# Kernel optimization log

Hardware: AMD Instinct MI355X
Metric: run time of the kernel (lower is better)

## Reference

```python
import jax, jax.numpy as jnp
import numpy as np

B, T, S = 16, 300, 160
N_MELS, PRE, ENC, ATT, LOC, K, DIM = 80, 256, 512, 128, 32, 31, 1024


def setup_inputs() -> dict:
    key = jax.random.key(0)
    ks = jax.random.split(key, 26)

    def rn(k, shape, fan_in):
        return (jax.random.normal(k, shape) / np.sqrt(fan_in)).astype(jnp.float32)

    inp = {}
    inp['mels'] = jax.random.normal(ks[0], (B, N_MELS, T), dtype=jnp.float32)
    inp['enc_out'] = jax.random.normal(ks[1], (B, S, ENC), dtype=jnp.float32)
    inp['text_len'] = jax.random.randint(ks[2], (B,), S // 2, S + 1).astype(jnp.int32)
    # attention params
    inp['Wt'] = rn(ks[3], (ATT, ENC), ENC)          # lin_target
    inp['Wq'] = rn(ks[4], (ATT, DIM), DIM)          # lin_query
    inp['w_score'] = rn(ks[5], (ATT,), ATT)         # lin_score weight [1,ATT] -> vector
    inp['conv1'] = rn(ks[6], (LOC, 1, K), K)        # Conv1d(1, loc_dim, K)
    inp['conv2'] = rn(ks[7], (ATT, LOC, 1), LOC)    # Conv1d(loc_dim, ATT, 1)
    # prenet (1x1 convs == per-frame linears)
    inp['pW1'] = rn(ks[8], (PRE, N_MELS), N_MELS)
    inp['pb1'] = jnp.zeros((PRE,), jnp.float32)
    inp['pW2'] = rn(ks[9], (PRE, PRE), PRE)
    inp['pb2'] = jnp.zeros((PRE,), jnp.float32)
    # 2-layer LSTM cells (gate order i,f,g,o as in torch)
    inp['Wih0'] = rn(ks[10], (4 * DIM, PRE + ENC), PRE + ENC)
    inp['Whh0'] = rn(ks[11], (4 * DIM, DIM), DIM)
    inp['bih0'] = jnp.zeros((4 * DIM,), jnp.float32)
    inp['bhh0'] = jnp.zeros((4 * DIM,), jnp.float32)
    inp['Wih1'] = rn(ks[12], (4 * DIM, DIM), DIM)
    inp['Whh1'] = rn(ks[13], (4 * DIM, DIM), DIM)
    inp['bih1'] = jnp.zeros((4 * DIM,), jnp.float32)
    inp['bhh1'] = jnp.zeros((4 * DIM,), jnp.float32)
    inp['h0'] = (jax.random.normal(ks[14], (2, DIM)) * 0.05).astype(jnp.float32)
    inp['c0'] = (jax.random.normal(ks[15], (2, DIM)) * 0.05).astype(jnp.float32)
    # projection
    inp['projW'] = rn(ks[16], (N_MELS + 1, ENC + DIM), ENC + DIM)
    inp['projb'] = jnp.zeros((N_MELS + 1,), jnp.float32)
    return inp


def _lstm_cell(x, h, c, Wih, Whh, bih, bhh):
    g = x @ Wih.T + bih + h @ Whh.T + bhh
    i, f, gg, o = jnp.split(g, 4, axis=-1)
    c2 = jax.nn.sigmoid(f) * c + jax.nn.sigmoid(i) * jnp.tanh(gg)
    h2 = jax.nn.sigmoid(o) * jnp.tanh(c2)
    return h2, c2


def reference(mels, enc_out, text_len, Wt, Wq, w_score, conv1, conv2,
              pW1, pb1, pW2, pb2,
              Wih0, Whh0, bih0, bhh0, Wih1, Whh1, bih1, bhh1,
              h0, c0, projW, projb):
    Bv, n_mel, Tv = mels.shape
    Sv = enc_out.shape[1]
    Kv = conv1.shape[-1]
    # prenet over [go, mels] (dropout disabled: deterministic=True, eval)
    mels_cat = jnp.concatenate([jnp.zeros((Bv, n_mel, 1), mels.dtype), mels], axis=2)
    p = jax.nn.relu(jnp.einsum('od,bdt->bot', pW1, mels_cat) + pb1[None, :, None])
    p = jax.nn.relu(jnp.einsum('od,bot->bot'.replace('o','q',1).replace('d','o').replace('q','o',1), pW2, p) + pb2[None, :, None]) if False else jax.nn.relu(jnp.einsum('od,bdt->bot', pW2, p) + pb2[None, :, None])
    mel_pre = jnp.transpose(p[:, :, :Tv], (2, 0, 1))  # [T, B, PRE]
    l_enc = enc_out @ Wt.T  # [B, S, ATT]
    pad_mask = jnp.arange(Sv)[None, :] >= text_len[:, None]  # [B, S] True at pads

    def step(carry, mel_t):
        h0_, h1_, c0_, c1_, cum = carry
        # location features from cumulative attention [B, S]
        loc = jax.lax.conv_general_dilated(cum[:, None, :], conv1, (1,),
                                           [(Kv // 2, Kv // 2)],
                                           dimension_numbers=('NCH', 'OIH', 'NCH'))  # [B,LOC,S]
        loc = jnp.einsum('al,bls->bsa', conv2[:, :, 0], loc)  # [B, S, ATT]
        q = h1_ @ Wq.T  # [B, ATT]
        score = jnp.tanh(q[:, None, :] + l_enc + loc) @ w_score  # [B, S]
        score = jnp.where(pad_mask, -jnp.inf, score)
        attn = jax.nn.softmax(score, axis=1)  # [B, S]
        align = jnp.einsum('bs,bse->be', attn, enc_out)  # [B, ENC]
        x = jnp.concatenate([mel_t, align], axis=1)
        h0n, c0n = _lstm_cell(x, h0_, c0_, Wih0, Whh0, bih0, bhh0)
        h1n, c1n = _lstm_cell(h0n, h1_, c1_, Wih1, Whh1, bih1, bhh1)
        cell_out = jnp.concatenate([h1n, align], axis=1)
        return (h0n, h1n, c0n, c1n, cum + attn), (cell_out, attn)

    init = (jnp.broadcast_to(h0[0], (Bv, h0.shape[1])),
            jnp.broadcast_to(h0[1], (Bv, h0.shape[1])),
            jnp.broadcast_to(c0[0], (Bv, c0.shape[1])),
            jnp.broadcast_to(c0[1], (Bv, c0.shape[1])),
            jnp.zeros((Bv, Sv), mels.dtype))
    _, (cell_outs, attns) = jax.lax.scan(step, init, mel_pre)
    proj = cell_outs @ projW.T + projb  # [T, B, n_mel+1]
    mel_out = jnp.transpose(proj[..., :n_mel], (1, 2, 0))   # [B, n_mel, T]
    stop_out = jnp.transpose(proj[..., n_mel], (1, 0))      # [B, T]
    attn_scores = jnp.transpose(attns, (1, 2, 0))           # [B, S, T]
    return mel_out, stop_out, attn_scores
```

## Files before the change

kernel.cpp:

```cpp
#include <hip/hip_runtime.h>

#define T_    300
#define B_    16
#define S_    160
#define NMEL_ 80
#define PRE_  256
#define ENC_  512
#define ATT_  128
#define DIM_  1024

#define XST1  1288
#define XST2  520
#define XST3  1032
#define AOFF  16512
#define WLDS  20608
#define XTOT  36992
#define BARWORDS 17408

#define HSLOT (B_*DIM_)
#define ASLOT (B_*ENC_)
#define GSLOT (B_*256)

typedef unsigned int u32;
typedef unsigned short u16;

__device__ __forceinline__ float fexp2f(float x) { return __builtin_amdgcn_exp2f(x); }
__device__ __forceinline__ float fsigf(float x)  { return 1.0f / (1.0f + fexp2f(-1.442695041f * x)); }
__device__ __forceinline__ float ftanhf(float x) {
  float xc = fminf(fmaxf(x, -15.0f), 15.0f);
  float e = fexp2f(2.885390082f * xc);
  return (e - 1.0f) / (e + 1.0f);
}

__device__ __forceinline__ u16 f2bf(float f) {
  u32 b = __float_as_uint(f);
  return (u16)((b + 0x7fffu + ((b >> 16) & 1u)) >> 16);
}
__device__ __forceinline__ float4 bf4(const u16* p) {
  const uint2 u = *(const uint2*)p;
  float4 w;
  w.x = __uint_as_float(u.x << 16);
  w.y = __uint_as_float(u.x & 0xffff0000u);
  w.z = __uint_as_float(u.y << 16);
  w.w = __uint_as_float(u.y & 0xffff0000u);
  return w;
}

__device__ __forceinline__ float4 ld1q_sys(const float* p) {
  float4 v;
  asm volatile("global_load_dwordx4 %0, %1, off sc0 sc1\n\ts_waitcnt vmcnt(0)"
               : "=v"(v) : "v"(p) : "memory");
  return v;
}
__device__ __forceinline__ void st_sys(float* p, float v) {
  asm volatile("global_store_dword %0, %1, off sc0 sc1" :: "v"(p), "v"(v) : "memory");
}
__device__ __forceinline__ u32 ld_sys_u32(const u32* p) {
  u32 r;
  asm volatile("global_load_dword %0, %1, off sc0 sc1\n\ts_waitcnt vmcnt(0)"
               : "=v"(r) : "v"(p) : "memory");
  return r;
}
__device__ __forceinline__ void st_sys_u32(u32* p, u32 v) {
  asm volatile("global_store_dword %0, %1, off sc0 sc1" :: "v"(p), "v"(v) : "memory");
}

__device__ __forceinline__ void gridbar(u32* bar, int tid, int blk, u32 ep) {
  asm volatile("s_waitcnt vmcnt(0)" ::: "memory");
  __syncthreads();
  if (tid == 0) {
    const int g = blk & 15;
    u32* cnt  = bar + g*1024;
    u32* grel = bar + g*1024 + 64;
    u32* tcnt = bar + 16384;
    const u32 tgt = ep*16u + 15u;
    u32 old = __hip_atomic_fetch_add(cnt, 1u, __ATOMIC_RELAXED, __HIP_MEMORY_SCOPE_AGENT);
    if (old == tgt) {
      u32 told = __hip_atomic_fetch_add(tcnt, 1u, __ATOMIC_RELAXED, __HIP_MEMORY_SCOPE_AGENT);
      if (told == tgt) {
        #pragma unroll
        for (int g2 = 0; g2 < 16; ++g2) st_sys_u32(bar + g2*1024 + 64, ep + 1u);
      } else {
        while (ld_sys_u32(grel) != ep + 1u) __builtin_amdgcn_s_sleep(1);
      }
    } else {
      while (ld_sys_u32(grel) != ep + 1u) __builtin_amdgcn_s_sleep(1);
    }
  }
  __syncthreads();
}

#define DPP_ADD(v, ctrl, rmask) do { \
  int _t = __builtin_amdgcn_update_dpp(0, __float_as_int(v), (ctrl), (rmask), 0xf, false); \
  (v) += __int_as_float(_t); } while (0)

#define REDUCE64(v) do { \
  DPP_ADD(v, 0x111, 0xf); \
  DPP_ADD(v, 0x112, 0xf); \
  DPP_ADD(v, 0x114, 0xf); \
  DPP_ADD(v, 0x118, 0xf); \
  DPP_ADD(v, 0x142, 0xa); \
  DPP_ADD(v, 0x143, 0x8); } while (0)

__launch_bounds__(256)
__global__ void prenet_kernel(const float* __restrict__ mels,
                              const float* __restrict__ pW1, const float* __restrict__ pb1,
                              const float* __restrict__ pW2, const float* __restrict__ pb2,
                              float* __restrict__ melpre) {
  __shared__ float mcol[NMEL_];
  __shared__ float pcol[PRE_];
  const int b = blockIdx.x / 30;
  const int tbase = (blockIdx.x % 30) * 10;
  const int tid = threadIdx.x;
  for (int f = 0; f < 10; ++f) {
    const int t = tbase + f;
    if (tid < NMEL_) mcol[tid] = (t == 0) ? 0.0f : mels[(b*NMEL_ + tid)*T_ + (t-1)];
    __syncthreads();
    {
      float a1 = pb1[tid];
      const float* w1 = pW1 + tid*NMEL_;
      for (int m = 0; m < NMEL_; ++m) a1 += w1[m]*mcol[m];
      pcol[tid] = fmaxf(a1, 0.0f);
    }
    __syncthreads();
    {
      float a2 = pb2[tid];
      const float* w2 = pW2 + tid*PRE_;
      for (int d = 0; d < PRE_; d += 4) {
        const float4 wv = *(const float4*)(w2 + d);
        a2 += wv.x*pcol[d] + wv.y*pcol[d+1] + wv.z*pcol[d+2] + wv.w*pcol[d+3];
      }
      melpre[(t*B_ + b)*PRE_ + tid] = fmaxf(a2, 0.0f);
    }
    __syncthreads();
  }
}

__launch_bounds__(256)
__global__ void init_kernel(const float* __restrict__ h0,
                            const float* __restrict__ conv1, const float* __restrict__ conv2,
                            float* __restrict__ h1buf, float* __restrict__ h0st,
                            float* __restrict__ weff, u32* __restrict__ bar) {
  const int idx = blockIdx.x*256 + threadIdx.x;
  if (idx < B_*DIM_) {
    const int j = idx & (DIM_-1);
    h0st[idx]  = h0[j];
    h1buf[idx] = h0[DIM_ + j];
  } else if (idx < B_*DIM_ + ATT_*32) {
    const int r = idx - B_*DIM_;
    const int a = r >> 5, k = r & 31;
    float acc = 0.0f;
    if (k < 31) {
      for (int l = 0; l < 32; ++l) acc += conv2[a*32 + l]*conv1[l*31 + k];
    }
    weff[r] = acc;
  } else if (idx < B_*DIM_ + ATT_*32 + BARWORDS) {
    bar[idx - (B_*DIM_ + ATT_*32)] = 0u;
  }
}

__launch_bounds__(256)
__global__ void wcvt_kernel(const float* __restrict__ Wih0, const float* __restrict__ Whh0,
                            const float* __restrict__ Wih1, const float* __restrict__ Whh1,
                            const float* __restrict__ Wq,
                            u16* __restrict__ Wih0h, u16* __restrict__ Whh0h,
                            u16* __restrict__ Wih1h, u16* __restrict__ Whh1h,
                            u16* __restrict__ Wqh) {
  const int n0 = 4096*768, n1 = 4096*1024, nq = ATT_*DIM_;
  const int stride = gridDim.x*256;
  for (int i = blockIdx.x*256 + threadIdx.x; i < n0; i += stride) Wih0h[i] = f2bf(Wih0[i]);
  for (int i = blockIdx.x*256 + threadIdx.x; i < n1; i += stride) {
    Whh0h[i] = f2bf(Whh0[i]);
    Wih1h[i] = f2bf(Wih1[i]);
    Whh1h[i] = f2bf(Whh1[i]);
  }
  for (int i = blockIdx.x*256 + threadIdx.x; i < nq; i += stride) Wqh[i] = f2bf(Wq[i]);
}

__launch_bounds__(256)
__global__ void lenc_kernel(const float* __restrict__ enc, const float* __restrict__ Wt,
                            float* __restrict__ lencb) {
  __shared__ float es[4*ENC_];
  const int b = blockIdx.x / 40;
  const int s0 = (blockIdx.x % 40) * 4;
  const int tid = threadIdx.x;
  for (int idx = tid; idx < 4*ENC_; idx += 256) es[idx] = enc[(b*S_ + s0)*ENC_ + idx];
  __syncthreads();
  const int a = tid & 127, sh = tid >> 7;
  const float* w = Wt + a*ENC_;
  for (int p = 0; p < 2; ++p) {
    const int sl = sh*2 + p;
    const float* e = es + sl*ENC_;
    float acc = 0.0f;
    for (int j = 0; j < ENC_; j += 4) {
      const float4 wv = *(const float4*)(w + j);
      acc += wv.x*e[j] + wv.y*e[j+1] + wv.z*e[j+2] + wv.w*e[j+3];
    }
    lencb[(b*S_ + s0 + sl)*ATT_ + a] = acc;
  }
}

__launch_bounds__(512, 1)
__global__ void decoder_kernel(
    const float* __restrict__ melpre, const float* __restrict__ lencb,
    const float* __restrict__ weff,
    float* __restrict__ h1buf, float* __restrict__ albuf, float* __restrict__ h0st,
    float* __restrict__ g0pre, float* __restrict__ g1pre, u32* __restrict__ bar,
    const float* __restrict__ enc, const int* __restrict__ tlen,
    const u16* __restrict__ Wqh, const float* __restrict__ wsc,
    const u16* __restrict__ Wih0h, const u16* __restrict__ Whh0h,
    const u16* __restrict__ Wih1h, const u16* __restrict__ Whh1h,
    const float* __restrict__ bih0, const float* __restrict__ bhh0,
    const float* __restrict__ bih1, const float* __restrict__ bhh1,
    const float* __restrict__ c0in, const float* __restrict__ projW, const float* __restrict__ projb,
    float* __restrict__ out_mel, float* __restrict__ out_stop, float* __restrict__ out_attn)
{
  extern __shared__ float xt[];
  __shared__ float red_s[1];
  __shared__ float gv[256];
  __shared__ float gv0[256];
  __shared__ float gv1[256];
  __shared__ float q_s[ATT_];
  __shared__ float spf[S_*4];
  __shared__ float score_s[S_];
  __shared__ float attn_s[S_];
  __shared__ float bsum_s[2][20];

  float* const cum_p = xt + AOFF;
  float* const projx = xt + AOFF + 192;
  float* const wscs  = xt + AOFF + 1728;
  u16* const wl = (u16*)(xt + WLDS);

  const int blk = blockIdx.x;
  const int tid = threadIdx.x;
  const int ks = tid & 63;
  const int bgb = ((tid >> 6) & 1)*8;
  const int rg = tid >> 7;
  const int j0 = blk*4;
  const bool hg0 = (blk >= 16 && blk < 80);
  const bool hg1 = (blk >= 80 && blk < 144);
  const int jx0 = blk - 16;
  const int jx1 = blk - 80;

  float c0r = 0.0f, c1r = 0.0f;
  if (tid < 64) {
    const int j = j0 + (tid >> 4);
    c0r = c0in[j];
    c1r = c0in[DIM_ + j];
  }
  int mylen = 0;
  if (blk < B_) {
    mylen = tlen[blk];
    for (int i = tid; i < S_ + 30; i += 512) cum_p[i] = 0.0f;
    if (tid < ATT_) wscs[tid] = wsc[tid];
  } else {
    for (int i = tid; i < 8192; i += 512) {
      const int c = i >> 6, l = i & 63;
      const int m = c >> 6, cm = c & 63;
      const int ri = cm >> 4, rgw = (cm >> 2) & 3, q = cm & 3;
      const u16* src = (m ? Whh1h : Wih1h) + (ri*1024 + j0 + rgw)*1024 + q*256 + l*4;
      *(uint2*)(wl + c*256 + l*4) = *(const uint2*)src;
    }
    if (tid < 16) {
      const int ri = tid >> 2, rgw = tid & 3;
      const int n = ri*1024 + j0 + rgw;
      bsum_s[0][tid] = bih0[n] + bhh0[n];
      bsum_s[1][tid] = bih1[n] + bhh1[n];
    } else if (tid < 20) {
      const int rgw = tid - 16;
      const int n0 = rgw*1024 + ((jx0 < 64) ? jx0 : 0);
      const int n1 = rgw*1024 + (hg1 ? jx1 : 0);
      bsum_s[0][16 + rgw] = bih0[n0] + bhh0[n0];
      bsum_s[1][16 + rgw] = bih1[n1] + bhh1[n1];
    }
  }
  __syncthreads();

  u32 ep = 0;

  for (int t = 0; t < T_; ++t) {
    if (blk < B_) {
      const int b = blk;
      if (tid < 256) {
        *(float4*)(projx + tid*4) =
            *(const float4*)(h1buf + t*HSLOT + b*DIM_ + tid*4);
      } else if (tid < 384) {
        const int j = tid - 256;
        const int ap = (t > 0) ? (t-1) : 0;
        *(float4*)(projx + 1024 + j*4) =
            *(const float4*)(albuf + ap*ASLOT + b*ENC_ + j*4);
      }
      __syncthreads();
      {
        const int a = tid & 127, part = tid >> 7;
        const float* hp = projx + part*256;
        const u16* wq = Wqh + a*DIM_ + part*256;
        float acc = 0.0f;
        for (int j = 0; j < 256; j += 4) {
          const float4 wv = bf4(wq + j);
          const float4 hv = *(const float4*)(hp + j);
          acc += wv.x*hv.x + wv.y*hv.y + wv.z*hv.z + wv.w*hv.w;
        }
        spf[a*4 + part] = acc;
      }
      __syncthreads();
      if (tid < ATT_) q_s[tid] = spf[tid*4] + spf[tid*4+1] + spf[tid*4+2] + spf[tid*4+3];
      __syncthreads();
      {
        const int sl = tid & 127, ag = tid >> 7;
        const int a0 = ag*32;
        #pragma unroll
        for (int p = 0; p < 2; ++p) {
          const int s = sl + p*128;
          if (s < S_) {
            float cw[32];
            #pragma unroll
            for (int k = 0; k < 31; ++k) cw[k] = cum_p[s + k];
            cw[31] = 0.0f;
            const float* le = lencb + (b*S_ + s)*ATT_ + a0;
            const float* wr = weff + a0*32;
            float ps = 0.0f;
            for (int i4 = 0; i4 < 8; ++i4) {
              const float4 lev = *(const float4*)(le + i4*4);
              #pragma unroll
              for (int ii = 0; ii < 4; ++ii) {
                const int i = i4*4 + ii;
                const float4* wk4 = (const float4*)(wr + i*32);
                float loc = 0.0f;
                #pragma unroll
                for (int kq = 0; kq < 8; ++kq) {
                  const float4 wv = wk4[kq];
                  loc += wv.x*cw[kq*4+0] + wv.y*cw[kq*4+1] + wv.z*cw[kq*4+2] + wv.w*cw[kq*4+3];
                }
                const float lef = (ii==0)?lev.x:(ii==1)?lev.y:(ii==2)?lev.z:lev.w;
                ps += wscs[a0 + i]*ftanhf(q_s[a0 + i] + lef + loc);
              }
            }
            spf[s*4 + ag] = ps;
          }
        }
      }
      __syncthreads();
      if (tid < S_) {
        float sc = spf[tid*4] + spf[tid*4+1] + spf[tid*4+2] + spf[tid*4+3];
        if (tid >= mylen) sc = -1.0e30f;
        score_s[tid] = sc;
      }
      __syncthreads();
      if (tid < 64) {
        float m = -1.0e30f;
        for (int i = tid; i < S_; i += 64) m = fmaxf(m, score_s[i]);
        #pragma unroll
        for (int o = 32; o > 0; o >>= 1) m = fmaxf(m, __shfl_xor(m, o, 64));
        float sum = 0.0f;
        for (int i = tid; i < S_; i += 64) {
          const float e = fexp2f(1.442695041f*(score_s[i] - m));
          score_s[i] = e;
          sum += e;
        }
        #pragma unroll
        for (int o = 32; o > 0; o >>= 1) sum += __shfl_xor(sum, o, 64);
        if (tid == 0) red_s[0] = sum;
      }
      __syncthreads();
      {
        const float inv = 1.0f / red_s[0];
        if (tid < S_) {
          const float av = score_s[tid]*inv;
          attn_s[tid] = av;
          cum_p[15 + tid] += av;
          out_attn[(b*S_ + tid)*T_ + t] = av;
        }
      }
      __syncthreads();
      {
        const float* eb = enc + (b*S_)*ENC_ + tid;
        float acc = 0.0f;
        for (int s = 0; s < S_; ++s) acc += attn_s[s]*eb[s*ENC_];
        st_sys(albuf + t*ASLOT + b*ENC_ + tid, acc);
      }
    } else {
      for (int i = tid; i < 1024; i += 512) {
        float4 v = *(const float4*)(melpre + t*4096 + i*4);
        *(float4*)(xt + (i>>6)*XST1 + (i&63)*4) = v;
      }
      {
        const float* src = h0st + t*HSLOT;
        float4 r[8];
        #pragma unroll
        for (int u = 0; u < 8; ++u) r[u] = *(const float4*)(src + (tid + u*512)*4);
        #pragma unroll
        for (int u = 0; u < 8; ++u) {
          const int i = tid + u*512;
          *(float4*)(xt + (i>>8)*XST1 + 256 + (i&255)*4) = r[u];
        }
      }
      __syncthreads();
      {
        const int nr = hg0 ? 5 : 4;
        int nrow[5];
        #pragma unroll
        for (int ri = 0; ri < 4; ++ri) nrow[ri] = ri*1024 + j0 + rg;
        nrow[4] = rg*1024 + ((jx0 < 64) ? jx0 : 0);
        #pragma unroll
        for (int hf = 0; hf < 2; ++hf) {
          const int b0 = bgb + hf*4;
          float acc[5][4];
          #pragma unroll
          for (int ri = 0; ri < 5; ++ri)
            #pragma unroll
            for (int bi = 0; bi < 4; ++bi) acc[ri][bi] = 0.0f;
          {
            const int j = ks*4;
            float4 w4[5];
            #pragma unroll
            for (int ri = 0; ri < 5; ++ri)
              if (ri < nr) w4[ri] = bf4(Wih0h + nrow[ri]*768 + j);
            #pragma unroll
            for (int bi = 0; bi < 4; ++bi) {
              const float4 xv = *(const float4*)(xt + (b0+bi)*XST1 + j);
              #pragma unroll
              for (int ri = 0; ri < 5; ++ri)
                if (ri < nr)
                  acc[ri][bi] += w4[ri].x*xv.x + w4[ri].y*xv.y + w4[ri].z*xv.z + w4[ri].w*xv.w;
            }
          }
          #pragma unroll
          for (int q = 0; q < 4; ++q) {
            const int j = q*256 + ks*4;
            float4 w4[5];
            #pragma unroll
            for (int ri = 0; ri < 5; ++ri)
              if (ri < nr) w4[ri] = bf4(Whh0h + nrow[ri]*1024 + j);
            #pragma unroll
            for (int bi = 0; bi < 4; ++bi) {
              const float4 xv = *(const float4*)(xt + (b0+bi)*XST1 + 256 + j);
              #pragma unroll
              for (int ri = 0; ri < 5; ++ri)
                if (ri < nr)
                  acc[ri][bi] += w4[ri].x*xv.x + w4[ri].y*xv.y + w4[ri].z*xv.z + w4[ri].w*xv.w;
            }
          }
          #pragma unroll
          for (int ri = 0; ri < 5; ++ri)
            if (ri < nr)
              #pragma unroll
              for (int bi = 0; bi < 4; ++bi) {
                float v = acc[ri][bi];
                REDUCE64(v);
                if (ks == 63) {
                  v += (ri < 4) ? bsum_s[0][ri*4 + rg] : bsum_s[0][16 + rg];
                  if (ri < 4) gv0[(ri*4 + rg)*16 + (b0+bi)] = v;
                  else        st_sys(g0pre + t*GSLOT + (b0+bi)*256 + jx0*4 + rg, v);
                }
              }
        }
      }
      __syncthreads();
      {
        const float* src = h1buf + t*HSLOT;
        float4 r[8];
        #pragma unroll
        for (int u = 0; u < 8; ++u) r[u] = *(const float4*)(src + (tid + u*512)*4);
        #pragma unroll
        for (int u = 0; u < 8; ++u) {
          const int i = tid + u*512;
          *(float4*)(xt + (i>>8)*XST1 + (i&255)*4) = r[u];
        }
      }
      __syncthreads();
      {
        const int nr = hg1 ? 5 : 4;
        const int nprox = rg*1024 + (hg1 ? jx1 : 0);
        #pragma unroll
        for (int hf = 0; hf < 2; ++hf) {
          const int b0 = bgb + hf*4;
          float acc[5][4];
          #pragma unroll
          for (int ri = 0; ri < 5; ++ri)
            #pragma unroll
            for (int bi = 0; bi < 4; ++bi) acc[ri][bi] = 0.0f;
          #pragma unroll
          for (int q = 0; q < 4; ++q) {
            const int j = q*256 + ks*4;
            float4 w4[5];
            #pragma unroll
            for (int ri = 0; ri < 4; ++ri)
              w4[ri] = bf4(wl + (64 + (ri*4 + rg)*4 + q)*256 + ks*4);
            if (nr == 5) w4[4] = bf4(Whh1h + nprox*1024 + j);
            #pragma unroll
            for (int bi = 0; bi < 4; ++bi) {
              const float4 xv = *(const float4*)(xt + (b0+bi)*XST1 + j);
              #pragma unroll
              for (int ri = 0; ri < 5; ++ri)
                if (ri < nr)
                  acc[ri][bi] += w4[ri].x*xv.x + w4[ri].y*xv.y + w4[ri].z*xv.z + w4[ri].w*xv.w;
            }
          }
          #pragma unroll
          for (int ri = 0; ri < 5; ++ri)
            if (ri < nr)
              #pragma unroll
              for (int bi = 0; bi < 4; ++bi) {
                float v = acc[ri][bi];
                REDUCE64(v);
                if (ks == 63) {
                  v += (ri < 4) ? bsum_s[1][ri*4 + rg] : bsum_s[1][16 + rg];
                  if (ri < 4) gv1[(ri*4 + rg)*16 + (b0+bi)] = v;
                  else        st_sys(g1pre + t*GSLOT + (b0+bi)*256 + jx1*4 + rg, v);
                }
              }
        }
      }
    }
    gridbar(bar, tid, blk, ep); ++ep;

    {
      {
        const float* src = albuf + t*ASLOT;
        float4 r[4];
        #pragma unroll
        for (int u = 0; u < 4; ++u) r[u] = *(const float4*)(src + (tid + u*512)*4);
        #pragma unroll
        for (int u = 0; u < 4; ++u) {
          const int i = tid + u*512;
          *(float4*)(xt + (i>>7)*XST2 + (i&127)*4) = r[u];
        }
      }
      __syncthreads();
      float acc[4][8];
      #pragma unroll
      for (int ri = 0; ri < 4; ++ri)
        #pragma unroll
        for (int bi = 0; bi < 8; ++bi) acc[ri][bi] = 0.0f;
      #pragma unroll
      for (int q = 0; q < 2; ++q) {
        const int j = q*256 + ks*4;
        float4 w4[4];
        #pragma unroll
        for (int ri = 0; ri < 4; ++ri)
          w4[ri] = bf4(Wih0h + (ri*1024 + j0 + rg)*768 + 256 + j);
        #pragma unroll
        for (int bi = 0; bi < 8; ++bi) {
          const float4 xv = *(const float4*)(xt + (bgb+bi)*XST2 + j);
          #pragma unroll
          for (int ri = 0; ri < 4; ++ri)
            acc[ri][bi] += w4[ri].x*xv.x + w4[ri].y*xv.y + w4[ri].z*xv.z + w4[ri].w*xv.w;
        }
      }
      #pragma unroll
      for (int ri = 0; ri < 4; ++ri)
        #pragma unroll
        for (int bi = 0; bi < 8; ++bi) {
          float v = acc[ri][bi];
          REDUCE64(v);
          if (ks == 63) gv[(rg*4 + ri)*16 + (bgb+bi)] = v;
        }
      __syncthreads();
      if (tid < 64) {
        const int jl = tid >> 4, bb = tid & 15;
        const int j = j0 + jl;
        float pi, pf, pg, po;
        if (blk < B_) {
          const float4 g4 = *(const float4*)(g0pre + t*GSLOT + bb*256 + j*4);
          pi = g4.x; pf = g4.y; pg = g4.z; po = g4.w;
        } else {
          pi = gv0[(0*4 + jl)*16 + bb];
          pf = gv0[(1*4 + jl)*16 + bb];
          pg = gv0[(2*4 + jl)*16 + bb];
          po = gv0[(3*4 + jl)*16 + bb];
        }
        const float gi = gv[(jl*4+0)*16 + bb] + pi;
        const float gf = gv[(jl*4+1)*16 + bb] + pf;
        const float gg = gv[(jl*4+2)*16 + bb] + pg;
        const float go = gv[(jl*4+3)*16 + bb] + po;
        const float cn = fsigf(gf)*c0r + fsigf(gi)*ftanhf(gg);
        const float hn = fsigf(go)*ftanhf(cn);
        c0r = cn;
        st_sys(h0st + (t+1)*HSLOT + bb*DIM_ + j, hn);
      }
    }
    gridbar(bar, tid, blk, ep); ++ep;

    {
      {
        const float* src = h0st + (t+1)*HSLOT;
        float4 r[8];
        #pragma unroll
        for (int u = 0; u < 8; ++u) r[u] = *(const float4*)(src + (tid + u*512)*4);
        #pragma unroll
        for (int u = 0; u < 8; ++u) {
          const int i = tid + u*512;
          *(float4*)(xt + (i>>8)*XST3 + (i&255)*4) = r[u];
        }
      }
      __syncthreads();
      float acc[4][8];
      #pragma unroll
      for (int ri = 0; ri < 4; ++ri)
        #pragma unroll
        for (int bi = 0; bi < 8; ++bi) acc[ri][bi] = 0.0f;
      #pragma unroll
      for (int q = 0; q < 4; ++q) {
        const int j = q*256 + ks*4;
        float4 w4[4];
        if (blk < B_) {
          #pragma unroll
          for (int ri = 0; ri < 4; ++ri)
            w4[ri] = bf4(Wih1h + (ri*1024 + j0 + rg)*1024 + j);
        } else {
          #pragma unroll
          for (int ri = 0; ri < 4; ++ri)
            w4[ri] = bf4(wl + (((ri*4 + rg)*4 + q) << 8) + ks*4);
        }
        #pragma unroll
        for (int bi = 0; bi < 8; ++bi) {
          const float4 xv = *(const float4*)(xt + (bgb+bi)*XST3 + j);
          #pragma unroll
          for (int ri = 0; ri < 4; ++ri)
            acc[ri][bi] += w4[ri].x*xv.x + w4[ri].y*xv.y + w4[ri].z*xv.z + w4[ri].w*xv.w;
        }
      }
      #pragma unroll
      for (int ri = 0; ri < 4; ++ri)
        #pragma unroll
        for (int bi = 0; bi < 8; ++bi) {
          float v = acc[ri][bi];
          REDUCE64(v);
          if (ks == 63) gv[(rg*4 + ri)*16 + (bgb+bi)] = v;
        }
      __syncthreads();
      if (tid < 64) {
        const int jl = tid >> 4, bb = tid & 15;
        const int j = j0 + jl;
        float pi, pf, pg, po;
        if (blk < B_) {
          const float4 g4 = *(const float4*)(g1pre + t*GSLOT + bb*256 + j*4);
          pi = g4.x; pf = g4.y; pg = g4.z; po = g4.w;
        } else {
          pi = gv1[(0*4 + jl)*16 + bb];
          pf = gv1[(1*4 + jl)*16 + bb];
          pg = gv1[(2*4 + jl)*16 + bb];
          po = gv1[(3*4 + jl)*16 + bb];
        }
        const float gi = gv[(jl*4+0)*16 + bb] + pi;
        const float gf = gv[(jl*4+1)*16 + bb] + pf;
        const float gg = gv[(jl*4+2)*16 + bb] + pg;
        const float go = gv[(jl*4+3)*16 + bb] + po;
        const float cn = fsigf(gf)*c1r + fsigf(gi)*ftanhf(gg);
        const float hn = fsigf(go)*ftanhf(cn);
        c1r = cn;
        st_sys(h1buf + (t+1)*HSLOT + bb*DIM_ + j, hn);
      }
      if (blk < B_ && t > 0) {
        const int b = blk;
        const int o = tid >> 2, part = tid & 3;
        if (o < 81) {
          const float* w = projW + o*1536;
          const int jb = part*384;
          float acc2 = 0.0f;
          for (int j = jb; j < jb + 384; j += 4) {
            const float4 wv = *(const float4*)(w + j);
            const float4 xv = *(const float4*)(projx + j);
            acc2 += wv.x*xv.x + wv.y*xv.y + wv.z*xv.z + wv.w*xv.w;
          }
          spf[o*4 + part] = acc2;
        }
        __syncthreads();
        if (tid < 81) {
          const float v = projb[tid] + spf[tid*4] + spf[tid*4+1] + spf[tid*4+2] + spf[tid*4+3];
          if (tid < 80) out_mel[(b*NMEL_ + tid)*T_ + (t-1)] = v;
          else          out_stop[b*T_ + (t-1)] = v;
        }
      }
    }
    gridbar(bar, tid, blk, ep); ++ep;
  }

  if (blk < B_) {
    const int b = blk;
    if (tid < 256) {
      *(float4*)(projx + tid*4) =
          *(const float4*)(h1buf + 300*HSLOT + b*DIM_ + tid*4);
    } else if (tid < 384) {
      const int j = tid - 256;
      *(float4*)(projx + 1024 + j*4) =
          *(const float4*)(albuf + 299*ASLOT + b*ENC_ + j*4);
    }
    __syncthreads();
    const int o = tid >> 2, part = tid & 3;
    if (o < 81) {
      const float* w = projW + o*1536;
      const int jb = part*384;
      float acc = 0.0f;
      for (int j = jb; j < jb + 384; j += 4) {
        const float4 wv = *(const float4*)(w + j);
        const float4 xv = *(const float4*)(projx + j);
        acc += wv.x*xv.x + wv.y*xv.y + wv.z*xv.z + wv.w*xv.w;
      }
      spf[o*4 + part] = acc;
    }
    __syncthreads();
    if (tid < 81) {
      const float v = projb[tid] + spf[tid*4] + spf[tid*4+1] + spf[tid*4+2] + spf[tid*4+3];
      if (tid < 80) out_mel[(b*NMEL_ + tid)*T_ + (T_-1)] = v;
      else          out_stop[b*T_ + (T_-1)] = v;
    }
  }
}

extern "C" void kernel_launch(void* const* d_in, const int* in_sizes, int n_in,
                              void* d_out, int out_size, void* d_ws, size_t ws_size,
                              hipStream_t stream) {
  const float* mels  = (const float*)d_in[0];
  const float* enc   = (const float*)d_in[1];
  const int*   tlen  = (const int*)d_in[2];
  const float* Wt    = (const float*)d_in[3];
  const float* Wq    = (const float*)d_in[4];
  const float* wsc   = (const float*)d_in[5];
  const float* conv1 = (const float*)d_in[6];
  const float* conv2 = (const float*)d_in[7];
  const float* pW1   = (const float*)d_in[8];
  const float* pb1   = (const float*)d_in[9];
  const float* pW2   = (const float*)d_in[10];
  const float* pb2   = (const float*)d_in[11];
  const float* Wih0  = (const float*)d_in[12];
  const float* Whh0  = (const float*)d_in[13];
  const float* bih0  = (const float*)d_in[14];
  const float* bhh0  = (const float*)d_in[15];
  const float* Wih1  = (const float*)d_in[16];
  const float* Whh1  = (const float*)d_in[17];
  const float* bih1  = (const float*)d_in[18];
  const float* bhh1  = (const float*)d_in[19];
  const float* h0    = (const float*)d_in[20];
  const float* c0    = (const float*)d_in[21];
  const float* projW = (const float*)d_in[22];
  const float* projb = (const float*)d_in[23];

  float* ws     = (float*)d_ws;
  float* melpre = ws;
  float* lencb  = melpre + 1228800;
  float* weff   = lencb + 327680;
  float* h1buf  = weff + 4096;
  float* albuf  = h1buf + 301*16384;
  float* h0st   = albuf + 300*8192;
  float* g0pre  = h0st + 301*16384;
  float* g1pre  = g0pre + 300*4096;
  u32*   bar    = (u32*)(g1pre + 300*4096);
  u16*   Wih0h  = (u16*)(bar + BARWORDS);
  u16*   Whh0h  = Wih0h + 4096*768;
  u16*   Wih1h  = Whh0h + 4096*1024;
  u16*   Whh1h  = Wih1h + 4096*1024;
  u16*   Wqh    = Whh1h + 4096*1024;

  float* out_mel  = (float*)d_out;
  float* out_stop = out_mel + 384000;
  float* out_attn = out_stop + 4800;

  prenet_kernel<<<dim3(480), dim3(256), 0, stream>>>(mels, pW1, pb1, pW2, pb2, melpre);
  init_kernel<<<dim3(160), dim3(256), 0, stream>>>(h0, conv1, conv2, h1buf, h0st, weff, bar);
  wcvt_kernel<<<dim3(2048), dim3(256), 0, stream>>>(Wih0, Whh0, Wih1, Whh1, Wq,
                                                    Wih0h, Whh0h, Wih1h, Whh1h, Wqh);
  lenc_kernel<<<dim3(640), dim3(256), 0, stream>>>(enc, Wt, lencb);

  void* args[] = {
    (void*)&melpre, (void*)&lencb, (void*)&weff, (void*)&h1buf, (void*)&albuf, (void*)&h0st,
    (void*)&g0pre, (void*)&g1pre, (void*)&bar,
    (void*)&enc, (void*)&tlen, (void*)&Wqh, (void*)&wsc,
    (void*)&Wih0h, (void*)&Whh0h, (void*)&Wih1h, (void*)&Whh1h,
    (void*)&bih0, (void*)&bhh0, (void*)&bih1, (void*)&bhh1,
    (void*)&c0, (void*)&projW, (void*)&projb,
    (void*)&out_mel, (void*)&out_stop, (void*)&out_attn
  };
  hipLaunchCooperativeKernel((const void*)decoder_kernel, dim3(256), dim3(512),
                             args, (unsigned int)(XTOT*sizeof(float)), stream);
}
```

Before: 30.54 ms.

## Replace full grid barriers with split arrive/wait and targeted flag waits

The first per-step grid barrier is replaced by targeted counters. One counter is signalled when the attention blocks finish, and another when the hg0 blocks finish their layer-0 partial sums. Consumers poll only the flag they need. The remaining barriers are split into arrive and wait halves, and independent work is moved into the gap between them: attention output stores, the output projection, and prefetching the next step's mel/h0/align inputs into LDS. This aims to cut barrier stall time per timestep, at the cost of more subtle cross-block ordering that could race if a dependency is missed.

```diff
diff --git a/kernel.cpp b/kernel.cpp
--- a/kernel.cpp
+++ b/kernel.cpp
@@ -65,13 +65,16 @@
   asm volatile("global_store_dword %0, %1, off sc0 sc1" :: "v"(p), "v"(v) : "memory");
 }
 
-__device__ __forceinline__ void gridbar(u32* bar, int tid, int blk, u32 ep) {
+__device__ __forceinline__ void poll_ge(const u32* p, u32 tgt) {
+  while ((int)(ld_sys_u32(p) - tgt) < 0) __builtin_amdgcn_s_sleep(1);
+}
+
+__device__ __forceinline__ void gb_arrive(u32* bar, int tid, int blk, u32 ep) {
   asm volatile("s_waitcnt vmcnt(0)" ::: "memory");
   __syncthreads();
   if (tid == 0) {
     const int g = blk & 15;
     u32* cnt  = bar + g*1024;
-    u32* grel = bar + g*1024 + 64;
     u32* tcnt = bar + 16384;
     const u32 tgt = ep*16u + 15u;
     u32 old = __hip_atomic_fetch_add(cnt, 1u, __ATOMIC_RELAXED, __HIP_MEMORY_SCOPE_AGENT);
@@ -80,12 +83,14 @@
       if (told == tgt) {
         #pragma unroll
         for (int g2 = 0; g2 < 16; ++g2) st_sys_u32(bar + g2*1024 + 64, ep + 1u);
-      } else {
-        while (ld_sys_u32(grel) != ep + 1u) __builtin_amdgcn_s_sleep(1);
-      }
-    } else {
-      while (ld_sys_u32(grel) != ep + 1u) __builtin_amdgcn_s_sleep(1);
-    }
+      }
+    }
+  }
+}
+__device__ __forceinline__ void gb_wait(u32* bar, int tid, int blk, u32 ep) {
+  if (tid == 0) {
+    const u32* grel = bar + (blk & 15)*1024 + 64;
+    poll_ge(grel, ep + 1u);
   }
   __syncthreads();
 }
@@ -242,6 +247,10 @@
   const int jx0 = blk - 16;
   const int jx1 = blk - 80;
 
+  u32* const attn_cnt = bar + 16384 + 128;
+  u32* const hg0_cnt  = bar + 16384 + 192;
+  u32* const hg0rel   = bar + 16384 + 256;
+
   float c0r = 0.0f, c1r = 0.0f;
   if (tid < 64) {
     const int j = j0 + (tid >> 4);
@@ -273,6 +282,14 @@
       bsum_s[0][16 + rgw] = bih0[n0] + bhh0[n0];
       bsum_s[1][16 + rgw] = bih1[n1] + bhh1[n1];
     }
+    for (int i = tid; i < 1024; i += 512) {
+      float4 v = *(const float4*)(melpre + i*4);
+      *(float4*)(xt + (i>>6)*XST1 + (i&63)*4) = v;
+    }
+    for (int u = 0; u < 8; ++u) {
+      const int i = tid + u*512;
+      *(float4*)(xt + (i>>8)*XST1 + 256 + (i&255)*4) = *(const float4*)(h0st + i*4);
+    }
   }
   __syncthreads();
 
@@ -284,11 +301,6 @@
       if (tid < 256) {
         *(float4*)(projx + tid*4) =
             *(const float4*)(h1buf + t*HSLOT + b*DIM_ + tid*4);
-      } else if (tid < 384) {
-        const int j = tid - 256;
-        const int ap = (t > 0) ? (t-1) : 0;
-        *(float4*)(projx + 1024 + j*4) =
-            *(const float4*)(albuf + ap*ASLOT + b*ENC_ + j*4);
       }
       __syncthreads();
       {
@@ -369,7 +381,6 @@
           const float av = score_s[tid]*inv;
           attn_s[tid] = av;
           cum_p[15 + tid] += av;
-          out_attn[(b*S_ + tid)*T_ + t] = av;
         }
       }
       __syncthreads();
@@ -379,23 +390,16 @@
         for (int s = 0; s < S_; ++s) acc += attn_s[s]*eb[s*ENC_];
         st_sys(albuf + t*ASLOT + b*ENC_ + tid, acc);
       }
+      asm volatile("s_waitcnt vmcnt(0)" ::: "memory");
+      __syncthreads();
+      if (tid == 0) {
+        u32 old = __hip_atomic_fetch_add(attn_cnt, 1u, __ATOMIC_RELAXED, __HIP_MEMORY_SCOPE_AGENT);
+        if (old == (u32)t*16u + 15u) {
+          #pragma unroll
+          for (int g2 = 0; g2 < 16; ++g2) st_sys_u32(bar + g2*1024 + 128, (u32)(t+1));
+        }
+      }
     } else {
-      for (int i = tid; i < 1024; i += 512) {
-        float4 v = *(const float4*)(melpre + t*4096 + i*4);
-        *(float4*)(xt + (i>>6)*XST1 + (i&63)*4) = v;
-      }
-      {
-        const float* src = h0st + t*HSLOT;
-        float4 r[8];
-        #pragma unroll
-        for (int u = 0; u < 8; ++u) r[u] = *(const float4*)(src + (tid + u*512)*4);
-        #pragma unroll
-        for (int u = 0; u < 8; ++u) {
-          const int i = tid + u*512;
-          *(float4*)(xt + (i>>8)*XST1 + 256 + (i&255)*4) = r[u];
-        }
-      }
-      __syncthreads();
       {
         const int nr = hg0 ? 5 : 4;
         int nrow[5];
@@ -456,7 +460,12 @@
               }
         }
       }
-      __syncthreads();
+      asm volatile("s_waitcnt vmcnt(0)" ::: "memory");
+      __syncthreads();
+      if (hg0 && tid == 0) {
+        u32 old = __hip_atomic_fetch_add(hg0_cnt, 1u, __ATOMIC_RELAXED, __HIP_MEMORY_SCOPE_AGENT);
+        if (old == (u32)t*64u + 63u) st_sys_u32(hg0rel, (u32)(t+1));
+      }
       {
         const float* src = h1buf + t*HSLOT;
         float4 r[8];
@@ -513,7 +522,8 @@
         }
       }
     }
-    gridbar(bar, tid, blk, ep); ++ep;
+    if (tid == 0) poll_ge(bar + (blk & 15)*1024 + 128, (u32)(t+1));
+    __syncthreads();
 
     {
       {
@@ -556,6 +566,7 @@
           REDUCE64(v);
           if (ks == 63) gv[(rg*4 + ri)*16 + (bgb+bi)] = v;
         }
+      if (blk < B_ && tid == 0) poll_ge(hg0rel, (u32)(t+1));
       __syncthreads();
       if (tid < 64) {
         const int jl = tid >> 4, bb = tid & 15;
@@ -580,7 +591,32 @@
         st_sys(h0st + (t+1)*HSLOT + bb*DIM_ + j, hn);
       }
     }
-    gridbar(bar, tid, blk, ep); ++ep;
+    gb_arrive(bar, tid, blk, ep);
+    if (blk < B_) {
+      const int b = blk;
+      if (tid < S_) out_attn[(b*S_ + tid)*T_ + t] = attn_s[tid];
+      if (t > 0) {
+        const int o = tid >> 2, part = tid & 3;
+        if (o < 81) {
+          const float* w = projW + o*1536;
+          const int jb = part*384;
+          float acc2 = 0.0f;
+          for (int j = jb; j < jb + 384; j += 4) {
+            const float4 wv = *(const float4*)(w + j);
+            const float4 xv = *(const float4*)(projx + j);
+            acc2 += wv.x*xv.x + wv.y*xv.y + wv.z*xv.z + wv.w*xv.w;
+          }
+          spf[o*4 + part] = acc2;
+        }
+        __syncthreads();
+        if (tid < 81) {
+          const float v = projb[tid] + spf[tid*4] + spf[tid*4+1] + spf[tid*4+2] + spf[tid*4+3];
+          if (tid < 80) out_mel[(b*NMEL_ + tid)*T_ + (t-1)] = v;
+          else          out_stop[b*T_ + (t-1)] = v;
+        }
+      }
+    }
+    gb_wait(bar, tid, blk, ep); ++ep;
 
     {
       {
@@ -652,29 +688,31 @@
         c1r = cn;
         st_sys(h1buf + (t+1)*HSLOT + bb*DIM_ + j, hn);
       }
-      if (blk < B_ && t > 0) {
-        const int b = blk;
-        const int o = tid >> 2, part = tid & 3;
-        if (o < 81) {
-          const float* w = projW + o*1536;
-          const int jb = part*384;
-          float acc2 = 0.0f;
-          for (int j = jb; j < jb + 384; j += 4) {
-            const float4 wv = *(const float4*)(w + j);
-            const float4 xv = *(const float4*)(projx + j);
-            acc2 += wv.x*xv.x + wv.y*xv.y + wv.z*xv.z + wv.w*xv.w;
-          }
-          spf[o*4 + part] = acc2;
-        }
-        __syncthreads();
-        if (tid < 81) {
-          const float v = projb[tid] + spf[tid*4] + spf[tid*4+1] + spf[tid*4+2] + spf[tid*4+3];
-          if (tid < 80) out_mel[(b*NMEL_ + tid)*T_ + (t-1)] = v;
-          else          out_stop[b*T_ + (t-1)] = v;
-        }
-      }
-    }
-    gridbar(bar, tid, blk, ep); ++ep;
+    }
+    gb_arrive(bar, tid, blk, ep);
+    if (t + 1 < T_) {
+      if (blk >= B_) {
+        for (int i = tid; i < 1024; i += 512) {
+          float4 v = *(const float4*)(melpre + (t+1)*4096 + i*4);
+          *(float4*)(xt + (i>>6)*XST1 + (i&63)*4) = v;
+        }
+        const float* src = h0st + (t+1)*HSLOT;
+        float4 r[8];
+        #pragma unroll
+        for (int u = 0; u < 8; ++u) r[u] = *(const float4*)(src + (tid + u*512)*4);
+        #pragma unroll
+        for (int u = 0; u < 8; ++u) {
+          const int i = tid + u*512;
+          *(float4*)(xt + (i>>8)*XST1 + 256 + (i&255)*4) = r[u];
+        }
+      } else {
+        if (tid < 128) {
+          *(float4*)(projx + 1024 + tid*4) =
+              *(const float4*)(albuf + t*ASLOT + blk*ENC_ + tid*4);
+        }
+      }
+    }
+    gb_wait(bar, tid, blk, ep); ++ep;
   }
 
   if (blk < B_) {
```

Measured after the change: 30.14 ms. About the same (-1.3%).
